# Kernel tuning notes

Hardware: AMD Instinct MI355X
Metric: run time of the kernel (lower is better)

Reference implementation:

```python
import jax, jax.numpy as jnp
import numpy as np

T, N, F, H, E = 12, 10000, 32, 64, 320000


def setup_inputs() -> dict:
    key = jax.random.key(0)
    ks = jax.random.split(key, 6)
    x = jax.random.normal(ks[0], (T, N, F), dtype=jnp.float32)
    edge_index = jax.random.randint(ks[1], (2, E), 0, N, dtype=jnp.int64)
    edge_weight = jax.random.uniform(ks[2], (E,), dtype=jnp.float32)
    missing_mask = jnp.ones((T, N, F), dtype=jnp.bool_)
    # GCNConv params (Glorot-ish init); PyG lin: out = x @ W, bias added after aggregation
    W1 = jax.random.normal(ks[3], (F, H), dtype=jnp.float32) * (1.0 / np.sqrt(F))
    b1 = jnp.zeros((H,), dtype=jnp.float32)
    W2 = jax.random.normal(ks[4], (H, F), dtype=jnp.float32) * (1.0 / np.sqrt(H))
    b2 = jnp.zeros((F,), dtype=jnp.float32)
    return dict(x=x, edge_index=edge_index, edge_weight=edge_weight,
                missing_mask=missing_mask, W1=W1, b1=b1, W2=W2, b2=b2)


def _gcn_norm(edge_weight, row, col, n_nodes):
    # PyG gcn_norm with add_self_loops=False: deg from dst, sym normalization
    deg = jax.ops.segment_sum(edge_weight, col, num_segments=n_nodes)
    dinv = jnp.where(deg > 0, 1.0 / jnp.sqrt(jnp.maximum(deg, 1e-12)), 0.0)
    return dinv[row] * edge_weight * dinv[col]


def _gcn_layer(h, row, col, norm, W, b):
    # h: (T, N, Fin) -> (T, N, Fout). Gather at src, weight, scatter-add at dst.
    h = h @ W                                   # (T, N, Fout)
    msg = h[:, row, :] * norm[None, :, None]    # (T, E, Fout)
    out = jnp.zeros((h.shape[0], h.shape[1], h.shape[2]), h.dtype)
    out = out.at[:, col, :].add(msg)
    return out + b


def reference(x, edge_index, edge_weight, missing_mask, W1, b1, W2, b2):
    n_nodes = x.shape[1]
    row, col = edge_index[0], edge_index[1]
    norm = _gcn_norm(edge_weight, row, col, n_nodes)
    h = _gcn_layer(x, row, col, norm, W1, b1)   # layer 0
    h = jax.nn.relu(h)                          # relu between layers
    h = _gcn_layer(h, row, col, norm, W2, b2)   # layer 1 (out_dim = in_dim)
    return jnp.tanh(h)                          # original returns (x, 0); we return x
```

## Files before the change

kernel.cpp:

```cpp
#include <hip/hip_runtime.h>
#include <hip/hip_fp16.h>

#define T_DIM   12
#define N_NODES 10000
#define F_IN    32
#define H_DIM   64
#define NCH     3
#define TC      4
#define CHROW   (TC * F_IN)
#define NGRP    (N_NODES / 16)
#define NTASK   (NCH * NGRP)
#define NROWS   (NCH * N_NODES * TC)
#define MROWS   128

#define CNT_SHIFT 40
#define FIX_SCALE 1048576.0f
#define FIX_MASK  ((1ull << CNT_SHIFT) - 1)

__global__ void zero_kernel(uint4* __restrict__ p, int n16) {
    int i = blockIdx.x * blockDim.x + threadIdx.x;
    if (i < n16) p[i] = make_uint4(0, 0, 0, 0);
}

__global__ void deg_hist_conv_kernel(const int* __restrict__ col,
                                     const float* __restrict__ w,
                                     unsigned long long* __restrict__ packed,
                                     unsigned int* __restrict__ posE, int E, int eb,
                                     const float* __restrict__ x,
                                     __half* __restrict__ xh) {
    int b = blockIdx.x;
    if (b < eb) {
        int e = b * 256 + threadIdx.x;
        if (e >= E) return;
        int c = col[e];
        unsigned long long fx = (unsigned long long)(w[e] * FIX_SCALE + 0.5f);
        unsigned long long old = atomicAdd(&packed[c], (1ull << CNT_SHIFT) | fx);
        posE[e] = (unsigned int)(old >> CNT_SHIFT);
    } else {
        int task = (b - eb) * 4 + (threadIdx.x >> 6);
        if (task >= NTASK) return;
        int l  = threadIdx.x & 63;
        int ch = task / NGRP;
        int ng = task - ch * NGRP;
        int n  = ng * 16 + (l >> 2);
        int t  = ch * TC + (l & 3);
        const float4* xp = (const float4*)(x + ((size_t)t * N_NODES + n) * F_IN);
        union { uint32_t u[16]; uint4 q[4]; } pk;
#pragma unroll
        for (int i = 0; i < 8; i++) {
            float4 v = xp[i];
            __half2 h0 = __floats2half2_rn(v.x, v.y);
            __half2 h1 = __floats2half2_rn(v.z, v.w);
            pk.u[2 * i]     = *(uint32_t*)&h0;
            pk.u[2 * i + 1] = *(uint32_t*)&h1;
        }
        uint4* dp = (uint4*)(xh + ((size_t)ch * N_NODES * TC + ng * 64 + l) * F_IN);
#pragma unroll
        for (int i = 0; i < 4; i++) dp[i] = pk.q[i];
    }
}

__global__ __launch_bounds__(1024) void scan_kernel(const unsigned long long* __restrict__ packed,
                                                    int* __restrict__ rowptr,
                                                    float* __restrict__ dinv, int n) {
    __shared__ int part[1024];
    int tid = threadIdx.x;
    const int per = (n + 1023) / 1024;
    int base = tid * per;
    int s = 0;
    for (int i = 0; i < per; i++) {
        int idx = base + i;
        if (idx < n) {
            unsigned long long p = packed[idx];
            s += (int)(p >> CNT_SHIFT);
            float deg = (float)(p & FIX_MASK) * (1.0f / FIX_SCALE);
            dinv[idx] = deg > 0.f ? rsqrtf(deg) : 0.f;
        }
    }
    part[tid] = s;
    __syncthreads();
    for (int off = 1; off < 1024; off <<= 1) {
        int v = 0;
        if (tid >= off) v = part[tid - off];
        __syncthreads();
        if (tid >= off) part[tid] += v;
        __syncthreads();
    }
    int run = (tid == 0) ? 0 : part[tid - 1];
    for (int i = 0; i < per; i++) {
        int idx = base + i;
        if (idx < n) {
            rowptr[idx] = run;
            run += (int)(packed[idx] >> CNT_SHIFT);
        }
    }
    if (tid == 1023) rowptr[n] = part[1023];
}

__global__ void fill_kernel(const int* __restrict__ row,
                            const int* __restrict__ col,
                            const float* __restrict__ w,
                            const float* __restrict__ dinv,
                            const int* __restrict__ rowptr,
                            const unsigned int* __restrict__ posE,
                            int2* __restrict__ edge_s, int E) {
    int e = blockIdx.x * blockDim.x + threadIdx.x;
    if (e >= E) return;
    int r = row[e];
    int c = col[e];
    float nw = dinv[r] * w[e] * dinv[c];
    int pos = rowptr[c] + (int)posE[e];
    edge_s[pos] = make_int2(r, __float_as_int(nw));
}

template <bool TANH>
__global__ __launch_bounds__(256) void gather64_kernel(const int* __restrict__ rowptr,
                                                       const int2* __restrict__ edge_s,
                                                       const __half* __restrict__ yh,
                                                       const float* __restrict__ bias,
                                                       float* __restrict__ outp, int n) {
    int c = blockIdx.x * 4 + (threadIdx.x >> 6);
    if (c >= n) return;
    int l    = threadIdx.x & 63;
    int half = l >> 5;
    int l32  = l & 31;

    int beg = rowptr[c], end = rowptr[c + 1];
    const __half* base = yh + 4 * l32;
    const size_t cstep = (size_t)N_NODES * CHROW;

    float4 a0 = {0.f, 0.f, 0.f, 0.f};
    float4 a1 = {0.f, 0.f, 0.f, 0.f};
    float4 a2 = {0.f, 0.f, 0.f, 0.f};

#pragma unroll 4
    for (int e = beg + half; e < end; e += 2) {
        int2 ed = edge_s[e];
        float nw = __int_as_float(ed.y);
        const __half* p = base + (size_t)ed.x * CHROW;
        uint2 u0 = *(const uint2*)(p);
        uint2 u1 = *(const uint2*)(p + cstep);
        uint2 u2 = *(const uint2*)(p + 2 * cstep);
        float2 f00 = __half22float2(*(__half2*)&u0.x), f01 = __half22float2(*(__half2*)&u0.y);
        float2 f10 = __half22float2(*(__half2*)&u1.x), f11 = __half22float2(*(__half2*)&u1.y);
        float2 f20 = __half22float2(*(__half2*)&u2.x), f21 = __half22float2(*(__half2*)&u2.y);
        a0.x = fmaf(f00.x, nw, a0.x); a0.y = fmaf(f00.y, nw, a0.y);
        a0.z = fmaf(f01.x, nw, a0.z); a0.w = fmaf(f01.y, nw, a0.w);
        a1.x = fmaf(f10.x, nw, a1.x); a1.y = fmaf(f10.y, nw, a1.y);
        a1.z = fmaf(f11.x, nw, a1.z); a1.w = fmaf(f11.y, nw, a1.w);
        a2.x = fmaf(f20.x, nw, a2.x); a2.y = fmaf(f20.y, nw, a2.y);
        a2.z = fmaf(f21.x, nw, a2.z); a2.w = fmaf(f21.y, nw, a2.w);
    }

    a0.x += __shfl_xor(a0.x, 32); a0.y += __shfl_xor(a0.y, 32);
    a0.z += __shfl_xor(a0.z, 32); a0.w += __shfl_xor(a0.w, 32);
    a1.x += __shfl_xor(a1.x, 32); a1.y += __shfl_xor(a1.y, 32);
    a1.z += __shfl_xor(a1.z, 32); a1.w += __shfl_xor(a1.w, 32);
    a2.x += __shfl_xor(a2.x, 32); a2.y += __shfl_xor(a2.y, 32);
    a2.z += __shfl_xor(a2.z, 32); a2.w += __shfl_xor(a2.w, 32);

    if (TANH) {
        float4 b4 = *(const float4*)(bias + 4 * (l32 & 7));
        if (half == 0) {
            a0.x = tanhf(a0.x + b4.x); a0.y = tanhf(a0.y + b4.y);
            a0.z = tanhf(a0.z + b4.z); a0.w = tanhf(a0.w + b4.w);
            a1.x = tanhf(a1.x + b4.x); a1.y = tanhf(a1.y + b4.y);
            a1.z = tanhf(a1.z + b4.z); a1.w = tanhf(a1.w + b4.w);
            int t0 = (l32 >> 3);
            float* op0 = outp + ((size_t)t0 * N_NODES + c) * F_IN + 4 * (l32 & 7);
            *(float4*)(op0)                               = a0;
            *(float4*)(op0 + (size_t)TC * N_NODES * F_IN) = a1;
        } else {
            a2.x = tanhf(a2.x + b4.x); a2.y = tanhf(a2.y + b4.y);
            a2.z = tanhf(a2.z + b4.z); a2.w = tanhf(a2.w + b4.w);
            int t2 = 2 * TC + (l32 >> 3);
            float* op2 = outp + ((size_t)t2 * N_NODES + c) * F_IN + 4 * (l32 & 7);
            *(float4*)op2 = a2;
        }
    } else {
        float* op = outp + (size_t)c * CHROW + 4 * l32;
        const size_t ostep = (size_t)N_NODES * CHROW;
        if (half == 0) {
            *(float4*)(op)         = a0;
            *(float4*)(op + ostep) = a1;
        } else {
            *(float4*)(op + 2 * ostep) = a2;
        }
    }
}

__global__ __launch_bounds__(128) void mlp_kernel(const float* __restrict__ aggx,
                                                  const float* __restrict__ W1g,
                                                  const float* __restrict__ b1,
                                                  const float* __restrict__ W2g,
                                                  __half* __restrict__ y2h) {
    __shared__ float W1s[F_IN * H_DIM];
    __shared__ float W2s[H_DIM * F_IN];
    __shared__ float b1s[H_DIM];
    __shared__ float xs[MROWS][F_IN + 1];
    __shared__ float hs[MROWS][H_DIM + 1];

    int tid = threadIdx.x;
    for (int i = tid; i < F_IN * H_DIM; i += 128) { W1s[i] = W1g[i]; W2s[i] = W2g[i]; }
    if (tid < H_DIM) b1s[tid] = b1[tid];

    size_t row0 = (size_t)blockIdx.x * MROWS;
    const float4* src = (const float4*)(aggx + row0 * F_IN);
    for (int i = tid; i < MROWS * (F_IN / 4); i += 128) {
        float4 v = src[i];
        int r = i >> 3, q = (i & 7) * 4;
        xs[r][q + 0] = v.x; xs[r][q + 1] = v.y; xs[r][q + 2] = v.z; xs[r][q + 3] = v.w;
    }
    __syncthreads();

    int rg = tid >> 2;
    int cg = tid & 3;
    int r0 = 4 * rg;

    {
        int c0 = 16 * cg;
        float acc[4][16];
#pragma unroll
        for (int j = 0; j < 16; j++) {
            float b = b1s[c0 + j];
#pragma unroll
            for (int rr = 0; rr < 4; rr++) acc[rr][j] = b;
        }
#pragma unroll 8
        for (int k = 0; k < F_IN; k++) {
            float xr[4];
#pragma unroll
            for (int rr = 0; rr < 4; rr++) xr[rr] = xs[r0 + rr][k];
#pragma unroll
            for (int j = 0; j < 16; j++) {
                float wv = W1s[k * H_DIM + c0 + j];
#pragma unroll
                for (int rr = 0; rr < 4; rr++) acc[rr][j] = fmaf(xr[rr], wv, acc[rr][j]);
            }
        }
#pragma unroll
        for (int rr = 0; rr < 4; rr++)
#pragma unroll
            for (int j = 0; j < 16; j++)
                hs[r0 + rr][c0 + j] = fmaxf(acc[rr][j], 0.f);
    }
    __syncthreads();

    {
        int d0 = 8 * cg;
        float acc[4][8];
#pragma unroll
        for (int rr = 0; rr < 4; rr++)
#pragma unroll
            for (int j = 0; j < 8; j++) acc[rr][j] = 0.f;
#pragma unroll 8
        for (int k = 0; k < H_DIM; k++) {
            float hr[4];
#pragma unroll
            for (int rr = 0; rr < 4; rr++) hr[rr] = hs[r0 + rr][k];
#pragma unroll
            for (int j = 0; j < 8; j++) {
                float wv = W2s[k * F_IN + d0 + j];
#pragma unroll
                for (int rr = 0; rr < 4; rr++) acc[rr][j] = fmaf(hr[rr], wv, acc[rr][j]);
            }
        }
#pragma unroll
        for (int rr = 0; rr < 4; rr++) {
            union { uint32_t u[4]; uint4 q; } pk;
#pragma unroll
            for (int i = 0; i < 4; i++) {
                __half2 hh = __floats2half2_rn(acc[rr][2 * i], acc[rr][2 * i + 1]);
                pk.u[i] = *(uint32_t*)&hh;
            }
            *(uint4*)(y2h + (row0 + r0 + rr) * F_IN + d0) = pk.q;
        }
    }
}

extern "C" void kernel_launch(void* const* d_in, const int* in_sizes, int n_in,
                              void* d_out, int out_size, void* d_ws, size_t ws_size,
                              hipStream_t stream) {
    const float* x  = (const float*)d_in[0];
    const int*   ei = (const int*)d_in[1];
    const float* w  = (const float*)d_in[2];
    const float* W1 = (const float*)d_in[4];
    const float* b1 = (const float*)d_in[5];
    const float* W2 = (const float*)d_in[6];
    const float* b2 = (const float*)d_in[7];
    float* out = (float*)d_out;

    const int E = in_sizes[1] / 2;
    const int* row = ei;
    const int* col = ei + E;

    char* ws = (char*)d_ws;
    size_t off = 0;
    auto alloc = [&](size_t bytes) { void* p = ws + off; off += (bytes + 255) & ~(size_t)255; return p; };
    unsigned long long* packed = (unsigned long long*)alloc(N_NODES * sizeof(unsigned long long));
    unsigned int* posE   = (unsigned int*)alloc((size_t)E * sizeof(unsigned int));
    int*    rowptr = (int*)   alloc((N_NODES + 1) * sizeof(int));
    float*  dinv   = (float*) alloc(N_NODES * sizeof(float));
    int2*   edge_s = (int2*)  alloc((size_t)E * sizeof(int2));
    __half* xh     = (__half*)alloc((size_t)NROWS * F_IN * sizeof(__half));
    __half* y2h    = (__half*)alloc((size_t)(NROWS + 64) * F_IN * sizeof(__half));
    float*  aggx   = (float*) alloc((size_t)(NROWS + 64) * F_IN * sizeof(float));

    const int eb = (E + 255) / 256;
    const int cb = (NTASK + 3) / 4;
    const int gb = (N_NODES + 3) / 4;
    const int mb = (NROWS + MROWS - 1) / MROWS;

    const int zn = (N_NODES * 8) / 16;
    zero_kernel<<<(zn + 255) / 256, 256, 0, stream>>>((uint4*)packed, zn);
    deg_hist_conv_kernel<<<eb + cb, 256, 0, stream>>>(col, w, packed, posE, E, eb, x, xh);
    scan_kernel<<<1, 1024, 0, stream>>>(packed, rowptr, dinv, N_NODES);
    fill_kernel<<<eb, 256, 0, stream>>>(row, col, w, dinv, rowptr, posE, edge_s, E);

    gather64_kernel<false><<<gb, 256, 0, stream>>>(rowptr, edge_s, xh, nullptr, aggx, N_NODES);
    mlp_kernel<<<mb, 128, 0, stream>>>(aggx, W1, b1, W2, y2h);

    gather64_kernel<true><<<gb, 256, 0, stream>>>(rowptr, edge_s, y2h, b2, out, N_NODES);
}
```

Measured before the change: 137.1 us.

## Store per-node timesteps contiguously and gather full 768-byte rows per edge

Changes the half-precision feature layout from three chunks of four timesteps to node-major storage, with all 12 timesteps of a node contiguous. The conversion and the intermediate aggregation buffers follow the same layout. The gather kernel now loads one 16-byte vector per lane covering a node's whole row in a single pass per edge, instead of three separate 256-byte chunk loads split across two half-waves. This aims to improve coalescing and cut address work per edge. The cost is 16 idle lanes doing duplicate loads, and each wave walking the edge list serially instead of two edges at a time.

```diff
diff --git a/kernel.cpp b/kernel.cpp
--- a/kernel.cpp
+++ b/kernel.cpp
@@ -5,13 +5,9 @@
 #define N_NODES 10000
 #define F_IN    32
 #define H_DIM   64
-#define NCH     3
-#define TC      4
-#define CHROW   (TC * F_IN)
-#define NGRP    (N_NODES / 16)
-#define NTASK   (NCH * NGRP)
-#define NROWS   (NCH * N_NODES * TC)
+#define NROWS   (N_NODES * T_DIM)
 #define MROWS   128
+#define NT8     (N_NODES / 8)
 
 #define CNT_SHIFT 40
 #define FIX_SCALE 1048576.0f
@@ -38,25 +34,30 @@
         posE[e] = (unsigned int)(old >> CNT_SHIFT);
     } else {
         int task = (b - eb) * 4 + (threadIdx.x >> 6);
-        if (task >= NTASK) return;
-        int l  = threadIdx.x & 63;
-        int ch = task / NGRP;
-        int ng = task - ch * NGRP;
-        int n  = ng * 16 + (l >> 2);
-        int t  = ch * TC + (l & 3);
-        const float4* xp = (const float4*)(x + ((size_t)t * N_NODES + n) * F_IN);
-        union { uint32_t u[16]; uint4 q[4]; } pk;
-#pragma unroll
-        for (int i = 0; i < 8; i++) {
-            float4 v = xp[i];
-            __half2 h0 = __floats2half2_rn(v.x, v.y);
-            __half2 h1 = __floats2half2_rn(v.z, v.w);
-            pk.u[2 * i]     = *(uint32_t*)&h0;
-            pk.u[2 * i + 1] = *(uint32_t*)&h1;
-        }
-        uint4* dp = (uint4*)(xh + ((size_t)ch * N_NODES * TC + ng * 64 + l) * F_IN);
-#pragma unroll
-        for (int i = 0; i < 4; i++) dp[i] = pk.q[i];
+        if (task >= NT8) return;
+        int l   = threadIdx.x & 63;
+        int nb8 = task * 8;
+#pragma unroll
+        for (int rep = 0; rep < 2; rep++) {
+            int r = rep * 64 + l;
+            if (rep == 1 && l >= 32) break;
+            int n_loc = r / 12;
+            int t     = r - 12 * n_loc;
+            int n     = nb8 + n_loc;
+            const float4* xp = (const float4*)(x + ((size_t)t * N_NODES + n) * F_IN);
+            union { uint32_t u[16]; uint4 q[4]; } pk;
+#pragma unroll
+            for (int i = 0; i < 8; i++) {
+                float4 v = xp[i];
+                __half2 h0 = __floats2half2_rn(v.x, v.y);
+                __half2 h1 = __floats2half2_rn(v.z, v.w);
+                pk.u[2 * i]     = *(uint32_t*)&h0;
+                pk.u[2 * i + 1] = *(uint32_t*)&h1;
+            }
+            uint4* dp = (uint4*)(xh + ((size_t)nb8 * T_DIM + r) * F_IN);
+#pragma unroll
+            for (int i = 0; i < 4; i++) dp[i] = pk.q[i];
+        }
     }
 }
 
@@ -114,77 +115,56 @@
 }
 
 template <bool TANH>
-__global__ __launch_bounds__(256) void gather64_kernel(const int* __restrict__ rowptr,
-                                                       const int2* __restrict__ edge_s,
-                                                       const __half* __restrict__ yh,
-                                                       const float* __restrict__ bias,
-                                                       float* __restrict__ outp, int n) {
+__global__ __launch_bounds__(256) void gatherV_kernel(const int* __restrict__ rowptr,
+                                                      const int2* __restrict__ edge_s,
+                                                      const __half* __restrict__ yh,
+                                                      const float* __restrict__ bias,
+                                                      float* __restrict__ outp, int n) {
     int c = blockIdx.x * 4 + (threadIdx.x >> 6);
     if (c >= n) return;
     int l    = threadIdx.x & 63;
-    int half = l >> 5;
-    int l32  = l & 31;
+    int lsel = (l < 48) ? l : (l - 48);
 
     int beg = rowptr[c], end = rowptr[c + 1];
-    const __half* base = yh + 4 * l32;
-    const size_t cstep = (size_t)N_NODES * CHROW;
-
-    float4 a0 = {0.f, 0.f, 0.f, 0.f};
-    float4 a1 = {0.f, 0.f, 0.f, 0.f};
-    float4 a2 = {0.f, 0.f, 0.f, 0.f};
+
+    float acc[8];
+#pragma unroll
+    for (int i = 0; i < 8; i++) acc[i] = 0.f;
 
 #pragma unroll 4
-    for (int e = beg + half; e < end; e += 2) {
+    for (int e = beg; e < end; e++) {
         int2 ed = edge_s[e];
         float nw = __int_as_float(ed.y);
-        const __half* p = base + (size_t)ed.x * CHROW;
-        uint2 u0 = *(const uint2*)(p);
-        uint2 u1 = *(const uint2*)(p + cstep);
-        uint2 u2 = *(const uint2*)(p + 2 * cstep);
-        float2 f00 = __half22float2(*(__half2*)&u0.x), f01 = __half22float2(*(__half2*)&u0.y);
-        float2 f10 = __half22float2(*(__half2*)&u1.x), f11 = __half22float2(*(__half2*)&u1.y);
-        float2 f20 = __half22float2(*(__half2*)&u2.x), f21 = __half22float2(*(__half2*)&u2.y);
-        a0.x = fmaf(f00.x, nw, a0.x); a0.y = fmaf(f00.y, nw, a0.y);
-        a0.z = fmaf(f01.x, nw, a0.z); a0.w = fmaf(f01.y, nw, a0.w);
-        a1.x = fmaf(f10.x, nw, a1.x); a1.y = fmaf(f10.y, nw, a1.y);
-        a1.z = fmaf(f11.x, nw, a1.z); a1.w = fmaf(f11.y, nw, a1.w);
-        a2.x = fmaf(f20.x, nw, a2.x); a2.y = fmaf(f20.y, nw, a2.y);
-        a2.z = fmaf(f21.x, nw, a2.z); a2.w = fmaf(f21.y, nw, a2.w);
-    }
-
-    a0.x += __shfl_xor(a0.x, 32); a0.y += __shfl_xor(a0.y, 32);
-    a0.z += __shfl_xor(a0.z, 32); a0.w += __shfl_xor(a0.w, 32);
-    a1.x += __shfl_xor(a1.x, 32); a1.y += __shfl_xor(a1.y, 32);
-    a1.z += __shfl_xor(a1.z, 32); a1.w += __shfl_xor(a1.w, 32);
-    a2.x += __shfl_xor(a2.x, 32); a2.y += __shfl_xor(a2.y, 32);
-    a2.z += __shfl_xor(a2.z, 32); a2.w += __shfl_xor(a2.w, 32);
-
-    if (TANH) {
-        float4 b4 = *(const float4*)(bias + 4 * (l32 & 7));
-        if (half == 0) {
-            a0.x = tanhf(a0.x + b4.x); a0.y = tanhf(a0.y + b4.y);
-            a0.z = tanhf(a0.z + b4.z); a0.w = tanhf(a0.w + b4.w);
-            a1.x = tanhf(a1.x + b4.x); a1.y = tanhf(a1.y + b4.y);
-            a1.z = tanhf(a1.z + b4.z); a1.w = tanhf(a1.w + b4.w);
-            int t0 = (l32 >> 3);
-            float* op0 = outp + ((size_t)t0 * N_NODES + c) * F_IN + 4 * (l32 & 7);
-            *(float4*)(op0)                               = a0;
-            *(float4*)(op0 + (size_t)TC * N_NODES * F_IN) = a1;
+        uint4 q = *((const uint4*)(yh + (size_t)ed.x * (T_DIM * F_IN)) + lsel);
+        const __half2* hh = (const __half2*)&q;
+#pragma unroll
+        for (int j = 0; j < 4; j++) {
+            float2 f = __half22float2(hh[j]);
+            acc[2 * j]     = fmaf(f.x, nw, acc[2 * j]);
+            acc[2 * j + 1] = fmaf(f.y, nw, acc[2 * j + 1]);
+        }
+    }
+
+    if (l < 48) {
+        int t  = l >> 2;
+        int f0 = (l & 3) * 8;
+        if (TANH) {
+            float4 blo = *(const float4*)(bias + f0);
+            float4 bhi = *(const float4*)(bias + f0 + 4);
+            float4 o0, o1;
+            o0.x = tanhf(acc[0] + blo.x); o0.y = tanhf(acc[1] + blo.y);
+            o0.z = tanhf(acc[2] + blo.z); o0.w = tanhf(acc[3] + blo.w);
+            o1.x = tanhf(acc[4] + bhi.x); o1.y = tanhf(acc[5] + bhi.y);
+            o1.z = tanhf(acc[6] + bhi.z); o1.w = tanhf(acc[7] + bhi.w);
+            float* op = outp + ((size_t)t * N_NODES + c) * F_IN + f0;
+            *(float4*)(op)     = o0;
+            *(float4*)(op + 4) = o1;
         } else {
-            a2.x = tanhf(a2.x + b4.x); a2.y = tanhf(a2.y + b4.y);
-            a2.z = tanhf(a2.z + b4.z); a2.w = tanhf(a2.w + b4.w);
-            int t2 = 2 * TC + (l32 >> 3);
-            float* op2 = outp + ((size_t)t2 * N_NODES + c) * F_IN + 4 * (l32 & 7);
-            *(float4*)op2 = a2;
-        }
-    } else {
-        float* op = outp + (size_t)c * CHROW + 4 * l32;
-        const size_t ostep = (size_t)N_NODES * CHROW;
-        if (half == 0) {
-            *(float4*)(op)         = a0;
-            *(float4*)(op + ostep) = a1;
-        } else {
-            *(float4*)(op + 2 * ostep) = a2;
+            float* op = outp + ((size_t)c * T_DIM + t) * F_IN + f0;
+            float4 o0 = {acc[0], acc[1], acc[2], acc[3]};
+            float4 o1 = {acc[4], acc[5], acc[6], acc[7]};
+            *(float4*)(op)     = o0;
+            *(float4*)(op + 4) = o1;
         }
     }
 }
@@ -298,7 +278,7 @@
     size_t off = 0;
     auto alloc = [&](size_t bytes) { void* p = ws + off; off += (bytes + 255) & ~(size_t)255; return p; };
     unsigned long long* packed = (unsigned long long*)alloc(N_NODES * sizeof(unsigned long long));
-    unsigned int* posE   = (unsigned int*)alloc((size_t)E * sizeof(unsigned int));
+    unsigned int* posE = (unsigned int*)alloc((size_t)E * sizeof(unsigned int));
     int*    rowptr = (int*)   alloc((N_NODES + 1) * sizeof(int));
     float*  dinv   = (float*) alloc(N_NODES * sizeof(float));
     int2*   edge_s = (int2*)  alloc((size_t)E * sizeof(int2));
@@ -307,7 +287,7 @@
     float*  aggx   = (float*) alloc((size_t)(NROWS + 64) * F_IN * sizeof(float));
 
     const int eb = (E + 255) / 256;
-    const int cb = (NTASK + 3) / 4;
+    const int cb = (NT8 + 3) / 4;
     const int gb = (N_NODES + 3) / 4;
     const int mb = (NROWS + MROWS - 1) / MROWS;
 
@@ -317,8 +297,8 @@
     scan_kernel<<<1, 1024, 0, stream>>>(packed, rowptr, dinv, N_NODES);
     fill_kernel<<<eb, 256, 0, stream>>>(row, col, w, dinv, rowptr, posE, edge_s, E);
 
-    gather64_kernel<false><<<gb, 256, 0, stream>>>(rowptr, edge_s, xh, nullptr, aggx, N_NODES);
+    gatherV_kernel<false><<<gb, 256, 0, stream>>>(rowptr, edge_s, xh, nullptr, aggx, N_NODES);
     mlp_kernel<<<mb, 128, 0, stream>>>(aggx, W1, b1, W2, y2h);
 
-    gather64_kernel<true><<<gb, 256, 0, stream>>>(rowptr, edge_s, y2h, b2, out, N_NODES);
-}
+    gatherV_kernel<true><<<gb, 256, 0, stream>>>(rowptr, edge_s, y2h, b2, out, N_NODES);
+}
```

Measured after the change: 137.5 us. No clear change (+0.3%).
